# Kernel optimization log

Hardware: AMD Instinct MI355X
Metric: run time of the kernel (lower is better)

## Reference

```python
import jax, jax.numpy as jnp
import numpy as np

CONF_THR = 0.5   # hard-coded `confidence` in pre_process_pred
NMS_THR = 0.5    # hard-coded `nms_conf` in pre_process_pred
IMG = 608.0


def setup_inputs() -> dict:
    key = jax.random.key(0)
    k1, k2, k3 = jax.random.split(key, 3)
    B, N, C = 16, 2048, 80
    u = jax.random.uniform(k1, (B, N, 4), dtype=jnp.float32)
    # cx, cy in [0, 608); w, h in [2, 120) pixels (YOLO-style pixel coords, matches +1 IoU convention)
    pred_boxes = jnp.concatenate([u[..., :2] * IMG, 2.0 + u[..., 2:] * 118.0], axis=-1)
    pred_objectness = jax.random.uniform(k2, (B, N, 1), dtype=jnp.float32)
    pred_logits = jax.random.uniform(k3, (B, N, C), dtype=jnp.float32)
    return {"pred_boxes": pred_boxes, "pred_objectness": pred_objectness, "pred_logits": pred_logits}


def _pairwise_iou(b):
    # b: [N,4] xyxy; +1 pixel convention exactly as original bbox_iou
    x1 = jnp.maximum(b[:, None, 0], b[None, :, 0])
    y1 = jnp.maximum(b[:, None, 1], b[None, :, 1])
    x2 = jnp.minimum(b[:, None, 2], b[None, :, 2])
    y2 = jnp.minimum(b[:, None, 3], b[None, :, 3])
    inter = jnp.clip(x2 - x1 + 1.0, 0.0) * jnp.clip(y2 - y1 + 1.0, 0.0)
    area = (b[:, 2] - b[:, 0] + 1.0) * (b[:, 3] - b[:, 1] + 1.0)
    return inter / (area[:, None] + area[None, :] - inter)


def _nms_one(boxes, obj, logits):
    # boxes: [N,4] cxcywh, obj: [N], logits: [N,C]
    N = boxes.shape[0]
    cx, cy, w, h = boxes[:, 0], boxes[:, 1], boxes[:, 2], boxes[:, 3]
    xyxy = jnp.stack([cx - w / 2, cy - h / 2, cx + w / 2, cy + h / 2], axis=-1)
    valid = obj > CONF_THR                    # confidence gate (strict >, as in original)
    cls_conf = jnp.max(logits, axis=-1)       # max_conf
    cls = jnp.argmax(logits, axis=-1)         # max_conf_score (class index)
    # sort by objectness descending; invalid boxes pushed to the end
    score = jnp.where(valid, obj, -jnp.inf)
    order = jnp.argsort(-score)
    xyxy_s = xyxy[order]
    obj_s = obj[order]
    valid_s = valid[order]
    cls_s = cls[order]
    conf_s = cls_conf[order]
    iou = _pairwise_iou(jax.lax.stop_gradient(xyxy_s))   # [N,N]
    same = cls_s[:, None] == cls_s[None, :]              # per-class NMS grouping
    idx = jnp.arange(N)

    def body(i, alive):
        # a box suppresses only if it is itself still alive & valid (greedy removal semantics)
        sup = alive[i] & valid_s[i] & (iou[i] >= NMS_THR) & same[i] & (idx > i)
        return alive & ~sup

    alive = jax.lax.fori_loop(0, N, body, valid_s)
    keep = alive & valid_s
    det = jnp.concatenate(
        [xyxy_s, obj_s[:, None], conf_s[:, None], cls_s.astype(xyxy_s.dtype)[:, None]], axis=-1
    )  # [N,7] = (x1,y1,x2,y2,obj,cls_conf,cls)
    return jnp.where(keep[:, None], det, 0.0)


def reference(pred_boxes, pred_objectness, pred_logits):
    obj = pred_objectness[..., 0]
    dets = jax.vmap(_nms_one)(pred_boxes, obj, pred_logits)  # [B,N,7]
    B, N, _ = dets.shape
    bind = jnp.broadcast_to(jnp.arange(B, dtype=dets.dtype)[:, None, None], (B, N, 1))
    # [B,N,8]: (batch_ind, x1,y1,x2,y2, obj, cls_conf, cls); suppressed rows are all-zero padding
    return jnp.concatenate([bind, dets], axis=-1)
```

## Files before the change

### kernel.cpp

```cpp
#include <hip/hip_runtime.h>
#include <stdint.h>

#define BB 16
#define NN 2048
#define CC 80
#define CONF_THRV 0.5f
#define NMS_THRV 0.5f

__global__ void k_classify(const float* __restrict__ logits,
                           const float* __restrict__ obj,
                           float* __restrict__ conf0,
                           int* __restrict__ cls0,
                           unsigned long long* __restrict__ keys) {
  int idx = blockIdx.x * blockDim.x + threadIdx.x;
  if (idx >= BB * NN) return;
  const float4* lp = (const float4*)(logits + (size_t)idx * CC);
  float best = -INFINITY;
  int bi = 0;
  #pragma unroll
  for (int q = 0; q < CC / 4; ++q) {
    float4 v = lp[q];
    if (v.x > best) { best = v.x; bi = 4 * q + 0; }
    if (v.y > best) { best = v.y; bi = 4 * q + 1; }
    if (v.z > best) { best = v.z; bi = 4 * q + 2; }
    if (v.w > best) { best = v.w; bi = 4 * q + 3; }
  }
  conf0[idx] = best;
  cls0[idx] = bi;
  float o = obj[idx];
  float s = (o > CONF_THRV) ? o : -INFINITY;
  unsigned u = __float_as_uint(s);
  u = (u & 0x80000000u) ? ~u : (u | 0x80000000u);
  unsigned n = (unsigned)(idx & (NN - 1));
  keys[idx] = ((unsigned long long)u << 32) | (unsigned long long)(0xFFFFFFFFu - n);
}

__global__ __launch_bounds__(1024) void k_sort_gather(
    const float4* __restrict__ boxes,
    const float* __restrict__ obj,
    const float* __restrict__ conf0,
    const int* __restrict__ cls0,
    const unsigned long long* __restrict__ keys,
    float4* __restrict__ sxyxy,
    float* __restrict__ sarea,
    float* __restrict__ sobj,
    float* __restrict__ sconf,
    int* __restrict__ scls,
    int* __restrict__ nvalid) {
  __shared__ unsigned long long sk[NN];
  __shared__ int cnt;
  int b = blockIdx.x;
  int t = threadIdx.x;
  if (t == 0) cnt = 0;
  size_t base = (size_t)b * NN;
  sk[t] = keys[base + t];
  sk[t + 1024] = keys[base + t + 1024];
  __syncthreads();
  for (unsigned k = 2; k <= NN; k <<= 1) {
    for (unsigned j = k >> 1; j > 0; j >>= 1) {
      #pragma unroll
      for (int rep = 0; rep < 2; ++rep) {
        unsigned e = (unsigned)t + (unsigned)rep * 1024u;
        unsigned ixj = e ^ j;
        if (ixj > e) {
          unsigned long long a = sk[e], c = sk[ixj];
          bool up = ((e & k) == 0);
          bool doswap = up ? (a < c) : (a > c);
          if (doswap) { sk[e] = c; sk[ixj] = a; }
        }
      }
      __syncthreads();
    }
  }
  int localvalid = 0;
  #pragma unroll
  for (int rep = 0; rep < 2; ++rep) {
    int e = t + rep * 1024;
    unsigned long long key = sk[e];
    unsigned id = 0xFFFFFFFFu - (unsigned)(key & 0xFFFFFFFFull);
    float4 bx = boxes[base + id];
    float hw = bx.z / 2.0f, hh = bx.w / 2.0f;
    float x1 = bx.x - hw, y1 = bx.y - hh;
    float x2 = bx.x + hw, y2 = bx.y + hh;
    float o = obj[base + id];
    sxyxy[base + e] = make_float4(x1, y1, x2, y2);
    sarea[base + e] = __fmul_rn(x2 - x1 + 1.0f, y2 - y1 + 1.0f);
    sobj[base + e] = o;
    sconf[base + e] = conf0[base + id];
    scls[base + e] = cls0[base + id];
    if (o > CONF_THRV) localvalid++;
  }
  atomicAdd(&cnt, localvalid);
  __syncthreads();
  if (t == 0) nvalid[b] = cnt;
}

__global__ void k_masks(const float4* __restrict__ sxyxy,
                        const float* __restrict__ sarea,
                        const int* __restrict__ scls,
                        const int* __restrict__ nvalid,
                        uint32_t* __restrict__ masksT) {
  int b = blockIdx.y;
  int pair = blockIdx.x * blockDim.x + threadIdx.x;
  int i = pair & (NN - 1);
  int w = pair >> 11;
  int nv = nvalid[b];
  size_t base = (size_t)b * NN;
  uint32_t bits = 0;
  int j0 = w * 32;
  int jend = min(j0 + 32, nv);
  int jstart = max(j0, i + 1);
  if (i < nv && jstart < jend) {
    float4 bi = sxyxy[base + i];
    float ai = sarea[base + i];
    int ci = scls[base + i];
    for (int j = jstart; j < jend; ++j) {
      float4 bj = sxyxy[base + j];
      float xx1 = fmaxf(bi.x, bj.x);
      float yy1 = fmaxf(bi.y, bj.y);
      float xx2 = fminf(bi.z, bj.z);
      float yy2 = fminf(bi.w, bj.w);
      float cw = fmaxf(xx2 - xx1 + 1.0f, 0.0f);
      float ch = fmaxf(yy2 - yy1 + 1.0f, 0.0f);
      float inter = __fmul_rn(cw, ch);
      float aj = sarea[base + j];
      float denom = (ai + aj) - inter;
      float iou = inter / denom;
      if (iou >= NMS_THRV && scls[base + j] == ci) bits |= (1u << (j - j0));
    }
  }
  masksT[((size_t)b * 64 + w) * NN + i] = bits;
}

__global__ __launch_bounds__(64) void k_scan(const uint32_t* __restrict__ masksT,
                                             uint32_t* __restrict__ remv_out) {
  int b = blockIdx.x;
  int lane = threadIdx.x;
  const uint4* col = (const uint4*)(masksT + ((size_t)b * 64 + lane) * NN);
  uint32_t remv = 0;
  uint4 A[8], B[8], C[8], D[8];
#define LOADBUF(BUF, CH) do {                                          \
    _Pragma("unroll")                                                  \
    for (int q = 0; q < 8; ++q) BUF[q] = col[(CH) * 8 + q];            \
  } while (0)
  LOADBUF(A, 0); LOADBUF(B, 1); LOADBUF(C, 2); LOADBUF(D, 3);
#define STEP(BUF, CH, RCH) do {                                        \
    uint32_t cur[32];                                                  \
    _Pragma("unroll")                                                  \
    for (int q = 0; q < 8; ++q) {                                      \
      cur[4*q+0] = BUF[q].x; cur[4*q+1] = BUF[q].y;                    \
      cur[4*q+2] = BUF[q].z; cur[4*q+3] = BUF[q].w;                    \
    }                                                                  \
    { int rr = (RCH) < 64 ? (RCH) : 0; LOADBUF(BUF, rr); }             \
    uint32_t all_or = 0;                                               \
    _Pragma("unroll")                                                  \
    for (int d = 0; d < 32; ++d) all_or |= cur[d];                     \
    uint32_t word_c = (uint32_t)__shfl((int)remv, (CH), 64);           \
    uint32_t diag   = (uint32_t)__shfl((int)all_or, (CH), 64);         \
    if (diag == 0u) {                                                  \
      if (word_c == 0u) {                                              \
        remv |= all_or;                         \
      } else {                                                         \
        uint32_t acc = 0;                                              \
        _Pragma("unroll")                                              \
        for (int d = 0; d < 32; ++d)                                   \
          acc |= ((word_c >> d) & 1u) ? 0u : cur[d];                   \
        remv |= acc;                                                   \
      }                                                                \
    } else {                                    \
      uint32_t wc = word_c, acc = 0;                                   \
      _Pragma("unroll")                                                \
      for (int d = 0; d < 32; ++d) {                                   \
        uint32_t dd = (uint32_t)__shfl((int)cur[d], (CH), 64);         \
        if (((wc >> d) & 1u) == 0u) { wc |= dd; acc |= cur[d]; }       \
      }                                                                \
      remv |= acc;                                                     \
    }                                                                  \
  } while (0)
  for (int c = 0; c < 64; c += 4) {
    STEP(A, c + 0, c + 4);
    STEP(B, c + 1, c + 5);
    STEP(C, c + 2, c + 6);
    STEP(D, c + 3, c + 7);
  }
#undef STEP
#undef LOADBUF
  remv_out[b * 64 + lane] = remv;
}

__global__ void k_write(const float4* __restrict__ sxyxy,
                        const float* __restrict__ sobj,
                        const float* __restrict__ sconf,
                        const int* __restrict__ scls,
                        const uint32_t* __restrict__ remv,
                        const int* __restrict__ nvalid,
                        float* __restrict__ out) {
  int idx = blockIdx.x * blockDim.x + threadIdx.x;
  if (idx >= BB * NN) return;
  int b = idx >> 11;
  int r = idx & (NN - 1);
  bool keep = false;
  if (r < nvalid[b]) {
    uint32_t wrd = remv[b * 64 + (r >> 5)];
    keep = !((wrd >> (r & 31)) & 1u);
  }
  float4 xy = make_float4(0.f, 0.f, 0.f, 0.f);
  float o = 0.f, cf = 0.f, cl = 0.f;
  if (keep) {
    xy = sxyxy[idx];
    o = sobj[idx];
    cf = sconf[idx];
    cl = (float)scls[idx];
  }
  float4* op = (float4*)(out + (size_t)idx * 8);
  op[0] = make_float4((float)b, xy.x, xy.y, xy.z);
  op[1] = make_float4(xy.w, o, cf, cl);
}

extern "C" void kernel_launch(void* const* d_in, const int* in_sizes, int n_in,
                              void* d_out, int out_size, void* d_ws, size_t ws_size,
                              hipStream_t stream) {
  const float4* boxes = (const float4*)d_in[0];
  const float* obj = (const float*)d_in[1];
  const float* logits = (const float*)d_in[2];
  float* out = (float*)d_out;

  char* ws = (char*)d_ws;
  size_t off = 0;
  float4* sxyxy = (float4*)(ws + off);            off += (size_t)BB * NN * 16;
  unsigned long long* keys = (unsigned long long*)(ws + off); off += (size_t)BB * NN * 8;
  float* conf0 = (float*)(ws + off);              off += (size_t)BB * NN * 4;
  int* cls0 = (int*)(ws + off);                   off += (size_t)BB * NN * 4;
  float* sarea = (float*)(ws + off);              off += (size_t)BB * NN * 4;
  float* sobj = (float*)(ws + off);               off += (size_t)BB * NN * 4;
  float* sconf = (float*)(ws + off);              off += (size_t)BB * NN * 4;
  int* scls = (int*)(ws + off);                   off += (size_t)BB * NN * 4;
  int* nvalid = (int*)(ws + off);                 off += 256;
  uint32_t* remv = (uint32_t*)(ws + off);         off += (size_t)BB * 64 * 4;
  uint32_t* masksT = (uint32_t*)(ws + off);       off += (size_t)BB * NN * 64 * 4;

  hipLaunchKernelGGL(k_classify, dim3((BB * NN + 255) / 256), dim3(256), 0, stream,
                     logits, obj, conf0, cls0, keys);
  hipLaunchKernelGGL(k_sort_gather, dim3(BB), dim3(1024), 0, stream,
                     boxes, obj, conf0, cls0, keys,
                     sxyxy, sarea, sobj, sconf, scls, nvalid);
  hipLaunchKernelGGL(k_masks, dim3(NN * 64 / 256, BB), dim3(256), 0, stream,
                     sxyxy, sarea, scls, nvalid, masksT);
  hipLaunchKernelGGL(k_scan, dim3(BB), dim3(64), 0, stream,
                     masksT, remv);
  hipLaunchKernelGGL(k_write, dim3((BB * NN + 255) / 256), dim3(256), 0, stream,
                     sxyxy, sobj, sconf, scls, remv, nvalid, out);
}
```

Before: 157.8 us.

## Fuse classify into sort kernel and scan into write kernel

Merges the per-box argmax/key-building pass into the per-batch sort kernel, keeping the keys and class results in shared memory, and merges the greedy bitmask scan with the output write into one kernel. This removes two launches and the global round-trips for keys, conf, cls and the removal words. The trade-off is that the 10 MB logits read now runs on only 16 blocks of 512 threads instead of a wide grid, so that stage may become bandwidth- or latency-limited. The sort block also shrinks from 1024 to 512 threads.

Measured after the change: 185.5 us. 1.18x slower.

```diff
diff --git a/kernel.cpp b/kernel.cpp
--- a/kernel.cpp
+++ b/kernel.cpp
@@ -7,40 +7,10 @@
 #define CONF_THRV 0.5f
 #define NMS_THRV 0.5f
 
-__global__ void k_classify(const float* __restrict__ logits,
-                           const float* __restrict__ obj,
-                           float* __restrict__ conf0,
-                           int* __restrict__ cls0,
-                           unsigned long long* __restrict__ keys) {
-  int idx = blockIdx.x * blockDim.x + threadIdx.x;
-  if (idx >= BB * NN) return;
-  const float4* lp = (const float4*)(logits + (size_t)idx * CC);
-  float best = -INFINITY;
-  int bi = 0;
-  #pragma unroll
-  for (int q = 0; q < CC / 4; ++q) {
-    float4 v = lp[q];
-    if (v.x > best) { best = v.x; bi = 4 * q + 0; }
-    if (v.y > best) { best = v.y; bi = 4 * q + 1; }
-    if (v.z > best) { best = v.z; bi = 4 * q + 2; }
-    if (v.w > best) { best = v.w; bi = 4 * q + 3; }
-  }
-  conf0[idx] = best;
-  cls0[idx] = bi;
-  float o = obj[idx];
-  float s = (o > CONF_THRV) ? o : -INFINITY;
-  unsigned u = __float_as_uint(s);
-  u = (u & 0x80000000u) ? ~u : (u | 0x80000000u);
-  unsigned n = (unsigned)(idx & (NN - 1));
-  keys[idx] = ((unsigned long long)u << 32) | (unsigned long long)(0xFFFFFFFFu - n);
-}
-
-__global__ __launch_bounds__(1024) void k_sort_gather(
+__global__ __launch_bounds__(512) void k_sort_all(
     const float4* __restrict__ boxes,
     const float* __restrict__ obj,
-    const float* __restrict__ conf0,
-    const int* __restrict__ cls0,
-    const unsigned long long* __restrict__ keys,
+    const float* __restrict__ logits,
     float4* __restrict__ sxyxy,
     float* __restrict__ sarea,
     float* __restrict__ sobj,
@@ -48,19 +18,44 @@
     int* __restrict__ scls,
     int* __restrict__ nvalid) {
   __shared__ unsigned long long sk[NN];
+  __shared__ float lconf[NN];
+  __shared__ int lcls[NN];
   __shared__ int cnt;
   int b = blockIdx.x;
   int t = threadIdx.x;
   if (t == 0) cnt = 0;
   size_t base = (size_t)b * NN;
-  sk[t] = keys[base + t];
-  sk[t + 1024] = keys[base + t + 1024];
+
+  #pragma unroll
+  for (int rep = 0; rep < 4; ++rep) {
+    int a = t + rep * 512;
+    const float4* lp = (const float4*)(logits + (base + a) * CC);
+    float best = -INFINITY;
+    int bi = 0;
+    #pragma unroll
+    for (int q = 0; q < CC / 4; ++q) {
+      float4 v = lp[q];
+      if (v.x > best) { best = v.x; bi = 4 * q + 0; }
+      if (v.y > best) { best = v.y; bi = 4 * q + 1; }
+      if (v.z > best) { best = v.z; bi = 4 * q + 2; }
+      if (v.w > best) { best = v.w; bi = 4 * q + 3; }
+    }
+    lconf[a] = best;
+    lcls[a] = bi;
+    float o = obj[base + a];
+    float s = (o > CONF_THRV) ? o : -INFINITY;
+    unsigned u = __float_as_uint(s);
+    u = (u & 0x80000000u) ? ~u : (u | 0x80000000u);
+    sk[a] = ((unsigned long long)u << 32) |
+            (unsigned long long)(0xFFFFFFFFu - (unsigned)a);
+  }
   __syncthreads();
+
   for (unsigned k = 2; k <= NN; k <<= 1) {
     for (unsigned j = k >> 1; j > 0; j >>= 1) {
       #pragma unroll
-      for (int rep = 0; rep < 2; ++rep) {
-        unsigned e = (unsigned)t + (unsigned)rep * 1024u;
+      for (int rep = 0; rep < 4; ++rep) {
+        unsigned e = (unsigned)t + (unsigned)rep * 512u;
         unsigned ixj = e ^ j;
         if (ixj > e) {
           unsigned long long a = sk[e], c = sk[ixj];
@@ -72,10 +67,11 @@
       __syncthreads();
     }
   }
+
   int localvalid = 0;
   #pragma unroll
-  for (int rep = 0; rep < 2; ++rep) {
-    int e = t + rep * 1024;
+  for (int rep = 0; rep < 4; ++rep) {
+    int e = t + rep * 512;
     unsigned long long key = sk[e];
     unsigned id = 0xFFFFFFFFu - (unsigned)(key & 0xFFFFFFFFull);
     float4 bx = boxes[base + id];
@@ -86,8 +82,8 @@
     sxyxy[base + e] = make_float4(x1, y1, x2, y2);
     sarea[base + e] = __fmul_rn(x2 - x1 + 1.0f, y2 - y1 + 1.0f);
     sobj[base + e] = o;
-    sconf[base + e] = conf0[base + id];
-    scls[base + e] = cls0[base + id];
+    sconf[base + e] = lconf[id];
+    scls[base + e] = lcls[id];
     if (o > CONF_THRV) localvalid++;
   }
   atomicAdd(&cnt, localvalid);
@@ -132,89 +128,95 @@
   masksT[((size_t)b * 64 + w) * NN + i] = bits;
 }
 
-__global__ __launch_bounds__(64) void k_scan(const uint32_t* __restrict__ masksT,
-                                             uint32_t* __restrict__ remv_out) {
+__global__ __launch_bounds__(512) void k_scan_write(
+    const uint32_t* __restrict__ masksT,
+    const int* __restrict__ nvalid,
+    const float4* __restrict__ sxyxy,
+    const float* __restrict__ sobj,
+    const float* __restrict__ sconf,
+    const int* __restrict__ scls,
+    float* __restrict__ out) {
+  __shared__ uint32_t rsh[64];
   int b = blockIdx.x;
-  int lane = threadIdx.x;
-  const uint4* col = (const uint4*)(masksT + ((size_t)b * 64 + lane) * NN);
-  uint32_t remv = 0;
-  uint4 A[8], B[8], C[8], D[8];
+  int t = threadIdx.x;
+
+  if (t < 64) {
+    int lane = t;
+    const uint4* col = (const uint4*)(masksT + ((size_t)b * 64 + lane) * NN);
+    uint32_t remv = 0;
+    uint4 A[8], B[8], C[8], D[8];
 #define LOADBUF(BUF, CH) do {                                          \
-    _Pragma("unroll")                                                  \
-    for (int q = 0; q < 8; ++q) BUF[q] = col[(CH) * 8 + q];            \
-  } while (0)
-  LOADBUF(A, 0); LOADBUF(B, 1); LOADBUF(C, 2); LOADBUF(D, 3);
+      _Pragma("unroll")                                                \
+      for (int q = 0; q < 8; ++q) BUF[q] = col[(CH) * 8 + q];          \
+    } while (0)
+    LOADBUF(A, 0); LOADBUF(B, 1); LOADBUF(C, 2); LOADBUF(D, 3);
 #define STEP(BUF, CH, RCH) do {                                        \
-    uint32_t cur[32];                                                  \
-    _Pragma("unroll")                                                  \
-    for (int q = 0; q < 8; ++q) {                                      \
-      cur[4*q+0] = BUF[q].x; cur[4*q+1] = BUF[q].y;                    \
-      cur[4*q+2] = BUF[q].z; cur[4*q+3] = BUF[q].w;                    \
-    }                                                                  \
-    { int rr = (RCH) < 64 ? (RCH) : 0; LOADBUF(BUF, rr); }             \
-    uint32_t all_or = 0;                                               \
-    _Pragma("unroll")                                                  \
-    for (int d = 0; d < 32; ++d) all_or |= cur[d];                     \
-    uint32_t word_c = (uint32_t)__shfl((int)remv, (CH), 64);           \
-    uint32_t diag   = (uint32_t)__shfl((int)all_or, (CH), 64);         \
-    if (diag == 0u) {                                                  \
-      if (word_c == 0u) {                                              \
-        remv |= all_or;                         \
+      uint32_t cur[32];                                                \
+      _Pragma("unroll")                                                \
+      for (int q = 0; q < 8; ++q) {                                    \
+        cur[4*q+0] = BUF[q].x; cur[4*q+1] = BUF[q].y;                  \
+        cur[4*q+2] = BUF[q].z; cur[4*q+3] = BUF[q].w;                  \
+      }                                                                \
+      { int rr = (RCH) < 64 ? (RCH) : 0; LOADBUF(BUF, rr); }           \
+      uint32_t all_or = 0;                                             \
+      _Pragma("unroll")                                                \
+      for (int d = 0; d < 32; ++d) all_or |= cur[d];                   \
+      uint32_t word_c = (uint32_t)__shfl((int)remv, (CH), 64);         \
+      uint32_t diag   = (uint32_t)__shfl((int)all_or, (CH), 64);       \
+      if (diag == 0u) {                                                \
+        if (word_c == 0u) {                                            \
+          remv |= all_or;                                              \
+        } else {                                                       \
+          uint32_t acc = 0;                                            \
+          _Pragma("unroll")                                            \
+          for (int d = 0; d < 32; ++d)                                 \
+            acc |= ((word_c >> d) & 1u) ? 0u : cur[d];                 \
+          remv |= acc;                                                 \
+        }                                                              \
       } else {                                                         \
-        uint32_t acc = 0;                                              \
+        uint32_t wc = word_c, acc = 0;                                 \
         _Pragma("unroll")                                              \
-        for (int d = 0; d < 32; ++d)                                   \
-          acc |= ((word_c >> d) & 1u) ? 0u : cur[d];                   \
+        for (int d = 0; d < 32; ++d) {                                 \
+          uint32_t dd = (uint32_t)__shfl((int)cur[d], (CH), 64);       \
+          if (((wc >> d) & 1u) == 0u) { wc |= dd; acc |= cur[d]; }     \
+        }                                                              \
         remv |= acc;                                                   \
       }                                                                \
-    } else {                                    \
-      uint32_t wc = word_c, acc = 0;                                   \
-      _Pragma("unroll")                                                \
-      for (int d = 0; d < 32; ++d) {                                   \
-        uint32_t dd = (uint32_t)__shfl((int)cur[d], (CH), 64);         \
-        if (((wc >> d) & 1u) == 0u) { wc |= dd; acc |= cur[d]; }       \
-      }                                                                \
-      remv |= acc;                                                     \
-    }                                                                  \
-  } while (0)
-  for (int c = 0; c < 64; c += 4) {
-    STEP(A, c + 0, c + 4);
-    STEP(B, c + 1, c + 5);
-    STEP(C, c + 2, c + 6);
-    STEP(D, c + 3, c + 7);
-  }
+    } while (0)
+    for (int c = 0; c < 64; c += 4) {
+      STEP(A, c + 0, c + 4);
+      STEP(B, c + 1, c + 5);
+      STEP(C, c + 2, c + 6);
+      STEP(D, c + 3, c + 7);
+    }
 #undef STEP
 #undef LOADBUF
-  remv_out[b * 64 + lane] = remv;
-}
-
-__global__ void k_write(const float4* __restrict__ sxyxy,
-                        const float* __restrict__ sobj,
-                        const float* __restrict__ sconf,
-                        const int* __restrict__ scls,
-                        const uint32_t* __restrict__ remv,
-                        const int* __restrict__ nvalid,
-                        float* __restrict__ out) {
-  int idx = blockIdx.x * blockDim.x + threadIdx.x;
-  if (idx >= BB * NN) return;
-  int b = idx >> 11;
-  int r = idx & (NN - 1);
-  bool keep = false;
-  if (r < nvalid[b]) {
-    uint32_t wrd = remv[b * 64 + (r >> 5)];
-    keep = !((wrd >> (r & 31)) & 1u);
-  }
-  float4 xy = make_float4(0.f, 0.f, 0.f, 0.f);
-  float o = 0.f, cf = 0.f, cl = 0.f;
-  if (keep) {
-    xy = sxyxy[idx];
-    o = sobj[idx];
-    cf = sconf[idx];
-    cl = (float)scls[idx];
-  }
-  float4* op = (float4*)(out + (size_t)idx * 8);
-  op[0] = make_float4((float)b, xy.x, xy.y, xy.z);
-  op[1] = make_float4(xy.w, o, cf, cl);
+    rsh[lane] = remv;
+  }
+  __syncthreads();
+
+  int nv = nvalid[b];
+  #pragma unroll
+  for (int rep = 0; rep < 4; ++rep) {
+    int r = t + rep * 512;
+    size_t idx = (size_t)b * NN + r;
+    bool keep = false;
+    if (r < nv) {
+      uint32_t wrd = rsh[r >> 5];
+      keep = !((wrd >> (r & 31)) & 1u);
+    }
+    float4 xy = make_float4(0.f, 0.f, 0.f, 0.f);
+    float o = 0.f, cf = 0.f, cl = 0.f;
+    if (keep) {
+      xy = sxyxy[idx];
+      o = sobj[idx];
+      cf = sconf[idx];
+      cl = (float)scls[idx];
+    }
+    float4* op = (float4*)(out + idx * 8);
+    op[0] = make_float4((float)b, xy.x, xy.y, xy.z);
+    op[1] = make_float4(xy.w, o, cf, cl);
+  }
 }
 
 extern "C" void kernel_launch(void* const* d_in, const int* in_sizes, int n_in,
@@ -228,26 +230,18 @@
   char* ws = (char*)d_ws;
   size_t off = 0;
   float4* sxyxy = (float4*)(ws + off);            off += (size_t)BB * NN * 16;
-  unsigned long long* keys = (unsigned long long*)(ws + off); off += (size_t)BB * NN * 8;
-  float* conf0 = (float*)(ws + off);              off += (size_t)BB * NN * 4;
-  int* cls0 = (int*)(ws + off);                   off += (size_t)BB * NN * 4;
   float* sarea = (float*)(ws + off);              off += (size_t)BB * NN * 4;
   float* sobj = (float*)(ws + off);               off += (size_t)BB * NN * 4;
   float* sconf = (float*)(ws + off);              off += (size_t)BB * NN * 4;
   int* scls = (int*)(ws + off);                   off += (size_t)BB * NN * 4;
   int* nvalid = (int*)(ws + off);                 off += 256;
-  uint32_t* remv = (uint32_t*)(ws + off);         off += (size_t)BB * 64 * 4;
   uint32_t* masksT = (uint32_t*)(ws + off);       off += (size_t)BB * NN * 64 * 4;
 
-  hipLaunchKernelGGL(k_classify, dim3((BB * NN + 255) / 256), dim3(256), 0, stream,
-                     logits, obj, conf0, cls0, keys);
-  hipLaunchKernelGGL(k_sort_gather, dim3(BB), dim3(1024), 0, stream,
-                     boxes, obj, conf0, cls0, keys,
+  hipLaunchKernelGGL(k_sort_all, dim3(BB), dim3(512), 0, stream,
+                     boxes, obj, logits,
                      sxyxy, sarea, sobj, sconf, scls, nvalid);
   hipLaunchKernelGGL(k_masks, dim3(NN * 64 / 256, BB), dim3(256), 0, stream,
                      sxyxy, sarea, scls, nvalid, masksT);
-  hipLaunchKernelGGL(k_scan, dim3(BB), dim3(64), 0, stream,
-                     masksT, remv);
-  hipLaunchKernelGGL(k_write, dim3((BB * NN + 255) / 256), dim3(256), 0, stream,
-                     sxyxy, sobj, sconf, scls, remv, nvalid, out);
-}
+  hipLaunchKernelGGL(k_scan_write, dim3(BB), dim3(512), 0, stream,
+                     masksT, nvalid, sxyxy, sobj, sconf, scls, out);
+}
```
